# Performance work log

Measured on AMD Instinct MI355X. Metric: run time of the kernel, lower is better.

The kernel has to match this reference:

```python
import jax, jax.numpy as jnp
import numpy as np

N_NODES = 100000
N_EDGES = 1600000
IN_CH = 128
HEADS = 4
OUT_CH = 32
EPS_BN = 1e-5


def setup_inputs() -> dict:
    key = jax.random.key(0)
    ks = jax.random.split(key, 8)
    s = 1.0 / np.sqrt(IN_CH)
    return {
        "x": jax.random.normal(ks[0], (N_NODES, IN_CH), jnp.float32),
        "edge_index": jax.random.randint(ks[1], (2, N_EDGES), 0, N_NODES, jnp.int32),
        "W_src": jax.random.normal(ks[2], (IN_CH, HEADS * OUT_CH), jnp.float32) * s,
        "W_dst": jax.random.normal(ks[3], (IN_CH, HEADS * OUT_CH), jnp.float32) * s,
        "att": jax.random.normal(ks[4], (HEADS, OUT_CH), jnp.float32) * s,
        "bias": jnp.zeros((HEADS * OUT_CH,), jnp.float32),
        "bn_gamma": jnp.ones((HEADS * OUT_CH,), jnp.float32),
        "bn_beta": jnp.zeros((HEADS * OUT_CH,), jnp.float32),
    }


def reference(x, edge_index, W_src, W_dst, att, bias, bn_gamma, bn_beta):
    N = x.shape[0]
    H, C = att.shape
    # add self-loops (PyG default add_self_loops=True)
    loop = jnp.arange(N, dtype=edge_index.dtype)
    src = jnp.concatenate([edge_index[0], loop])  # source j
    dst = jnp.concatenate([edge_index[1], loop])  # destination i

    h_src = (x @ W_src).reshape(N, H, C)
    h_dst = (x @ W_dst).reshape(N, H, C)

    # GATv2 edge scores: a^T LeakyReLU(h_src[j] + h_dst[i]), slope 0.2
    e = jax.nn.leaky_relu(h_src[src] + h_dst[dst], 0.2)  # [E+N, H, C]
    logits = jnp.einsum('ehc,hc->eh', e, att)            # [E+N, H]

    # segment softmax over incoming edges of each destination node
    m = jax.ops.segment_max(logits, dst, num_segments=N)  # [N, H]
    ex = jnp.exp(logits - m[dst])
    denom = jax.ops.segment_sum(ex, dst, num_segments=N)  # [N, H] (>0 via self-loops)
    alpha = ex / denom[dst]                                # [E+N, H]

    # weighted scatter-sum aggregation of source features
    out = jax.ops.segment_sum(alpha[:, :, None] * h_src[src], dst, num_segments=N)
    out = out.reshape(N, H * C) + bias

    # BatchNorm1d (training-mode batch statistics) + LeakyReLU(0.02)
    mean = out.mean(axis=0)
    var = out.var(axis=0)
    y = bn_gamma * (out - mean) * jax.lax.rsqrt(var + EPS_BN) + bn_beta
    return jax.nn.leaky_relu(y, 0.02)
```

## Files before the change

### kernel.cpp

```cpp
#include <hip/hip_runtime.h>
#include <math.h>

#define N_IN   128
#define HC     128
#define HEADS  4
#define PB_T   4096
#define PB_THR 512
#define CAP    8192
#define STB    1024

typedef __attribute__((ext_vector_type(2))) __fp16 f16x2;
typedef __attribute__((ext_vector_type(8))) __fp16 f16x8;
typedef __attribute__((ext_vector_type(4))) float f32x4;

__device__ __forceinline__ unsigned f16pk(float a, float b) {
    f16x2 r = __builtin_amdgcn_cvt_pkrtz(a, b);
    return __builtin_bit_cast(unsigned, r);
}

__global__ __launch_bounds__(256) void k_prep(const float* __restrict__ Ws,
        const float* __restrict__ Wd, unsigned short* __restrict__ Wt) {
    int i = blockIdx.x * 256 + threadIdx.x;
    if (i >= 256 * 128) return;
    int n = i >> 7, k = i & 127;
    float v = (n < 128) ? Ws[k * HC + n] : Wd[k * HC + (n - 128)];
    __fp16 h = (__fp16)v;
    Wt[i] = __builtin_bit_cast(unsigned short, h);
}

__global__ __launch_bounds__(256) void k_gemm(const float* __restrict__ x,
        const __fp16* __restrict__ Wt,
        unsigned short* __restrict__ hs, unsigned short* __restrict__ hd, int N) {
    int wave = threadIdx.x >> 6, lane = threadIdx.x & 63;
    int chbase = wave * 64;
    int nbase = blockIdx.x * 32;
    int lr = lane & 15;
    int lg = lane >> 4;

    f16x8 a[4][4];
#pragma unroll
    for (int ct = 0; ct < 4; ct++)
#pragma unroll
        for (int kk = 0; kk < 4; kk++)
            a[ct][kk] = *reinterpret_cast<const f16x8*>(
                &Wt[(size_t)(chbase + ct * 16 + lr) * 128 + kk * 32 + lg * 8]);

    f32x4 acc[2][4];
#pragma unroll
    for (int rt = 0; rt < 2; rt++)
#pragma unroll
        for (int ct = 0; ct < 4; ct++)
            acc[rt][ct] = (f32x4){0.f, 0.f, 0.f, 0.f};

#pragma unroll
    for (int rt = 0; rt < 2; rt++) {
        int node = nbase + rt * 16 + lr;
        const float* xr = x + (size_t)node * N_IN;
        bool ok = (node < N);
        f16x8 bfr[4];
#pragma unroll
        for (int kk = 0; kk < 4; kk++) {
            f32x4 xa = (f32x4){0.f, 0.f, 0.f, 0.f}, xb = xa;
            if (ok) {
                xa = *reinterpret_cast<const f32x4*>(xr + kk * 32 + lg * 8);
                xb = *reinterpret_cast<const f32x4*>(xr + kk * 32 + lg * 8 + 4);
            }
            uint4 u;
            u.x = f16pk(xa[0], xa[1]); u.y = f16pk(xa[2], xa[3]);
            u.z = f16pk(xb[0], xb[1]); u.w = f16pk(xb[2], xb[3]);
            bfr[kk] = __builtin_bit_cast(f16x8, u);
        }
#pragma unroll
        for (int kk = 0; kk < 4; kk++)
#pragma unroll
            for (int ct = 0; ct < 4; ct++)
                acc[rt][ct] = __builtin_amdgcn_mfma_f32_16x16x32_f16(
                    a[ct][kk], bfr[kk], acc[rt][ct], 0, 0, 0);
    }

#pragma unroll
    for (int rt = 0; rt < 2; rt++) {
        int node = nbase + rt * 16 + lr;
        if (node >= N) continue;
#pragma unroll
        for (int ct = 0; ct < 4; ct++) {
            int ch = chbase + ct * 16 + lg * 4;
            unsigned short* outp = (ch < HC) ? hs : hd;
            int cc = ch & (HC - 1);
            uint2 r;
            r.x = f16pk(acc[rt][ct][0], acc[rt][ct][1]);
            r.y = f16pk(acc[rt][ct][2], acc[rt][ct][3]);
            *reinterpret_cast<uint2*>(outp + (size_t)node * HC + cc) = r;
        }
    }
}

__global__ __launch_bounds__(PB_THR) void k_part(const int* __restrict__ ei,
        int* __restrict__ bcur, unsigned* __restrict__ ebuf, int E, int NB) {
    __shared__ int cnt[512], lscan[512], gbase[512], lcnt[512];
    __shared__ unsigned pr[PB_T];
    __shared__ unsigned short pb[PB_T];
    int t = threadIdx.x;
    int tb = blockIdx.x * PB_T;
    int tc = min(PB_T, E - tb);
    cnt[t] = 0; lcnt[t] = 0;
    __syncthreads();
    int dd[8], ss[8];
#pragma unroll
    for (int i = 0; i < 8; i++) {
        int e = tb + t + i * PB_THR;
        if (e < E) {
            ss[i] = ei[e];
            dd[i] = ei[E + e];
            atomicAdd(&cnt[dd[i] >> 8], 1);
        } else dd[i] = -1;
    }
    __syncthreads();
    lscan[t] = cnt[t];
    __syncthreads();
    for (int ofs = 1; ofs < 512; ofs <<= 1) {
        int add = (t >= ofs) ? lscan[t - ofs] : 0;
        __syncthreads();
        lscan[t] += add;
        __syncthreads();
    }
    if (t < NB && cnt[t] > 0) gbase[t] = atomicAdd(&bcur[t], cnt[t]);
    __syncthreads();
#pragma unroll
    for (int i = 0; i < 8; i++) {
        if (dd[i] >= 0) {
            int b = dd[i] >> 8;
            int lpos = atomicAdd(&lcnt[b], 1);
            int j = lscan[b] - cnt[b] + lpos;
            pr[j] = ((unsigned)ss[i] << 8) | (unsigned)(dd[i] & 255);
            pb[j] = (unsigned short)b;
        }
    }
    __syncthreads();
    for (int k = t; k < tc; k += PB_THR) {
        int b = pb[k];
        ebuf[(size_t)b * CAP + gbase[b] + k - (lscan[b] - cnt[b])] = pr[k];
    }
}

__global__ __launch_bounds__(256) void k_place(const unsigned* __restrict__ ebuf,
        const int* __restrict__ bcur, int* __restrict__ deg, int* __restrict__ off,
        int* __restrict__ ssrc, int N) {
    __shared__ int hist[256], loff[256];
    int b = blockIdx.x;
    int t = threadIdx.x;
    int base = b * CAP;
    int cntb = bcur[b];
    hist[t] = 0;
    __syncthreads();
    for (int k = t; k < cntb; k += 256)
        atomicAdd(&hist[ebuf[base + k] & 255u], 1);
    __syncthreads();
    int v = hist[t];
    loff[t] = v;
    __syncthreads();
    for (int ofs = 1; ofs < 256; ofs <<= 1) {
        int add = (t >= ofs) ? loff[t - ofs] : 0;
        __syncthreads();
        loff[t] += add;
        __syncthreads();
    }
    int excl = loff[t] - v;
    int node = (b << 8) + t;
    if (node < N) { deg[node] = v; off[node] = base + excl; }
    hist[t] = base + excl;
    __syncthreads();
    for (int k = t; k < cntb; k += 256) {
        unsigned u = ebuf[base + k];
        int pos = atomicAdd(&hist[u & 255u], 1);
        ssrc[pos] = (int)(u & 0xFFFFFF00u);
    }
}

__device__ __forceinline__ f16x2 ldh2(const unsigned short* p) {
    return __builtin_bit_cast(f16x2, *reinterpret_cast<const unsigned*>(p));
}
__device__ __forceinline__ f16x2 ldh2o(const unsigned char* b, unsigned o) {
    return __builtin_bit_cast(f16x2, *reinterpret_cast<const unsigned*>(b + o));
}
__device__ __forceinline__ float edge_logit(f16x2 v, f16x2 hdv, f16x2 at2) {
    f16x2 s = v + hdv;
    f16x2 g = s * (f16x2){(__fp16)0.2f, (__fp16)0.2f};
    f16x2 tt = __builtin_elementwise_max(s, g);
    float p = __builtin_amdgcn_fdot2(tt, at2, 0.f, false);
    p += __shfl_xor(p, 1); p += __shfl_xor(p, 2);
    p += __shfl_xor(p, 4); p += __shfl_xor(p, 8);
    return p;
}

__global__ __launch_bounds__(256) void k_agg2(const unsigned short* __restrict__ hs,
        const unsigned short* __restrict__ hd, const int* __restrict__ off,
        const int* __restrict__ deg, const int* __restrict__ ssrc,
        const float* __restrict__ att, unsigned* __restrict__ outh, int N) {
    int wid = (blockIdx.x * 256 + threadIdx.x) >> 6;
    int lane = threadIdx.x & 63;
    if (wid >= N) return;
    int c2 = lane * 2;
    unsigned c4 = (unsigned)lane * 4u;
    const unsigned char* hsb = (const unsigned char*)hs;
    float2 atf = *reinterpret_cast<const float2*>(&att[c2]);
    f16x2 at2 = {(__fp16)atf.x, (__fp16)atf.y};
    f16x2 hdv = ldh2(&hd[(size_t)wid * HC + c2]);
    f16x2 v = ldh2o(hsb, (unsigned)wid * 256u + c4);
    float p = edge_logit(v, hdv, at2);
    float e = __expf(p);
    float ssum = e;
    float2 acc = make_float2(e * (float)v[0], e * (float)v[1]);
    int beg = off[wid], end = beg + deg[wid];
    int i = beg;
    for (; i + 3 < end; i += 4) {
        unsigned o0 = (unsigned)ssrc[i]     + c4;
        unsigned o1 = (unsigned)ssrc[i + 1] + c4;
        unsigned o2 = (unsigned)ssrc[i + 2] + c4;
        unsigned o3 = (unsigned)ssrc[i + 3] + c4;
        f16x2 v0 = ldh2o(hsb, o0);
        f16x2 v1 = ldh2o(hsb, o1);
        f16x2 v2 = ldh2o(hsb, o2);
        f16x2 v3 = ldh2o(hsb, o3);
        float p0 = edge_logit(v0, hdv, at2);
        float p1 = edge_logit(v1, hdv, at2);
        float p2 = edge_logit(v2, hdv, at2);
        float p3 = edge_logit(v3, hdv, at2);
        float e0 = __expf(p0), e1 = __expf(p1);
        float e2 = __expf(p2), e3 = __expf(p3);
        ssum += (e0 + e1) + (e2 + e3);
        acc.x += e0 * (float)v0[0] + e1 * (float)v1[0]
               + e2 * (float)v2[0] + e3 * (float)v3[0];
        acc.y += e0 * (float)v0[1] + e1 * (float)v1[1]
               + e2 * (float)v2[1] + e3 * (float)v3[1];
    }
    for (; i < end; i++) {
        f16x2 ve = ldh2o(hsb, (unsigned)ssrc[i] + c4);
        float pe = edge_logit(ve, hdv, at2);
        float ee = __expf(pe);
        ssum += ee;
        acc.x += ee * (float)ve[0];
        acc.y += ee * (float)ve[1];
    }
    float inv = 1.f / ssum;
    outh[(size_t)wid * 64 + lane] = f16pk(acc.x * inv, acc.y * inv);
}

__global__ __launch_bounds__(256) void k_stats(const unsigned short* __restrict__ outh16,
        float* __restrict__ statp, int N) {
    int ch = threadIdx.x & 127;
    int half = threadIdx.x >> 7;
    float s = 0.f, s2 = 0.f;
    for (int n = blockIdx.x * 2 + half; n < N; n += gridDim.x * 2) {
        __fp16 h = __builtin_bit_cast(__fp16, outh16[(size_t)n * HC + ch]);
        float v = (float)h;
        s += v; s2 += v * v;
    }
    __shared__ float sh[2][256];
    sh[0][threadIdx.x] = s; sh[1][threadIdx.x] = s2;
    __syncthreads();
    if (threadIdx.x < 128) {
        size_t base = (size_t)blockIdx.x * 256;
        statp[base + threadIdx.x]       = sh[0][threadIdx.x] + sh[0][threadIdx.x + 128];
        statp[base + 128 + threadIdx.x] = sh[1][threadIdx.x] + sh[1][threadIdx.x + 128];
    }
}

__global__ __launch_bounds__(256) void k_redstats(const float* __restrict__ statp,
        float* __restrict__ stats, int NBLK) {
    int t = threadIdx.x;
    float acc = 0.f;
    for (int r = blockIdx.x; r < NBLK; r += gridDim.x)
        acc += statp[(size_t)r * 256 + t];
    atomicAdd(&stats[t], acc);
}

__global__ void k_bnparams(const float* __restrict__ stats,
        const float* __restrict__ gamma, const float* __restrict__ beta,
        float* __restrict__ ss, int N) {
    int c = threadIdx.x;
    if (c >= HC) return;
    float mean = stats[c] / (float)N;
    float var  = stats[HC + c] / (float)N - mean * mean;
    float sc = gamma[c] * rsqrtf(var + 1e-5f);
    ss[c]      = sc;
    ss[HC + c] = beta[c] - mean * sc;
}

__global__ __launch_bounds__(256) void k_final(const unsigned short* __restrict__ outh16,
        const float* __restrict__ ss, float* __restrict__ out, int total) {
    int i = blockIdx.x * 256 + threadIdx.x;
    if (i >= total) return;
    int c = i & 127;
    __fp16 h = __builtin_bit_cast(__fp16, outh16[i]);
    float y = (float)h * ss[c] + ss[HC + c];
    out[i] = (y > 0.f) ? y : 0.02f * y;
}

extern "C" void kernel_launch(void* const* d_in, const int* in_sizes, int n_in,
                              void* d_out, int out_size, void* d_ws, size_t ws_size,
                              hipStream_t stream) {
    const float* x     = (const float*)d_in[0];
    const int*   ei    = (const int*)d_in[1];
    const float* Ws    = (const float*)d_in[2];
    const float* Wd    = (const float*)d_in[3];
    const float* att   = (const float*)d_in[4];
    const float* gamma = (const float*)d_in[6];
    const float* beta  = (const float*)d_in[7];
    float* out = (float*)d_out;

    int N  = in_sizes[0] / N_IN;
    int E  = in_sizes[1] / 2;
    int NB = (N + 255) >> 8;

    char* ws = (char*)d_ws;
    unsigned short* hs = (unsigned short*)ws; ws += (size_t)N * HC * 2;
    unsigned short* hd = (unsigned short*)ws; ws += (size_t)N * HC * 2;
    unsigned* outh = (unsigned*)ws; ws += (size_t)N * HC * 2;
    int* deg    = (int*)ws;      ws += (size_t)N * 4;
    int* off    = (int*)ws;      ws += (size_t)N * 4;
    unsigned* ebuf = (unsigned*)ws; ws += (size_t)NB * CAP * 4;
    int* ssrc   = (int*)ws;      ws += (size_t)NB * CAP * 4;
    int* bcur   = (int*)ws;      ws += (size_t)NB * 4;
    unsigned short* Wt = (unsigned short*)ws; ws += 256 * 128 * 2;
    float* statp= (float*)ws;    ws += (size_t)STB * 256 * 4;
    float* stats= (float*)ws;    ws += 2 * HC * 4;
    float* ss   = (float*)ws;    ws += 2 * HC * 4;

    hipMemsetAsync(bcur, 0, (size_t)NB * 4, stream);
    hipMemsetAsync(stats, 0, 2 * HC * 4, stream);

    k_prep<<<128, 256, 0, stream>>>(Ws, Wd, Wt);
    k_gemm<<<(N + 31) / 32, 256, 0, stream>>>(x, (const __fp16*)Wt, hs, hd, N);
    k_part<<<(E + PB_T - 1) / PB_T, PB_THR, 0, stream>>>(ei, bcur, ebuf, E, NB);
    k_place<<<NB, 256, 0, stream>>>(ebuf, bcur, deg, off, ssrc, N);
    k_agg2<<<(N * 64 + 255) / 256, 256, 0, stream>>>(hs, hd, off, deg, ssrc, att, outh, N);
    k_stats<<<STB, 256, 0, stream>>>((const unsigned short*)outh, statp, N);
    k_redstats<<<64, 256, 0, stream>>>(statp, stats, STB);
    k_bnparams<<<1, 128, 0, stream>>>(stats, gamma, beta, ss, N);
    k_final<<<(N * HC + 255) / 256, 256, 0, stream>>>((const unsigned short*)outh, ss, out, N * HC);
}
```

Baseline: 240.2 us.

## Restructure GAT aggregation to split heads across blocks and parallelize edges within wave

```diff
diff --git a/kernel.cpp b/kernel.cpp
--- a/kernel.cpp
+++ b/kernel.cpp
@@ -177,73 +177,95 @@
     }
 }
 
-__device__ __forceinline__ f16x2 ldh2(const unsigned short* p) {
-    return __builtin_bit_cast(f16x2, *reinterpret_cast<const unsigned*>(p));
-}
-__device__ __forceinline__ f16x2 ldh2o(const unsigned char* b, unsigned o) {
-    return __builtin_bit_cast(f16x2, *reinterpret_cast<const unsigned*>(b + o));
-}
-__device__ __forceinline__ float edge_logit(f16x2 v, f16x2 hdv, f16x2 at2) {
-    f16x2 s = v + hdv;
-    f16x2 g = s * (f16x2){(__fp16)0.2f, (__fp16)0.2f};
-    f16x2 tt = __builtin_elementwise_max(s, g);
-    float p = __builtin_amdgcn_fdot2(tt, at2, 0.f, false);
-    p += __shfl_xor(p, 1); p += __shfl_xor(p, 2);
-    p += __shfl_xor(p, 4); p += __shfl_xor(p, 8);
-    return p;
-}
-
 __global__ __launch_bounds__(256) void k_agg2(const unsigned short* __restrict__ hs,
         const unsigned short* __restrict__ hd, const int* __restrict__ off,
         const int* __restrict__ deg, const int* __restrict__ ssrc,
-        const float* __restrict__ att, unsigned* __restrict__ outh, int N) {
-    int wid = (blockIdx.x * 256 + threadIdx.x) >> 6;
+        const float* __restrict__ att, unsigned* __restrict__ outh,
+        int N, int NP) {
+    int b = blockIdx.x;
+    int H = (b >> 2) & 1;
+    int j = (b >> 3) * 4 + (b & 3);
+    int pair = j * 4 + (threadIdx.x >> 6);
+    if (pair >= NP) return;
     int lane = threadIdx.x & 63;
-    if (wid >= N) return;
-    int c2 = lane * 2;
-    unsigned c4 = (unsigned)lane * 4u;
+    int g  = lane >> 5;
+    int e  = (lane >> 3) & 3;
+    int cb = lane & 7;
+    int node = pair * 2 + g;
+    if (node >= N) return;
+
+    unsigned rowoff = (unsigned)(H * 128 + cb * 16);
     const unsigned char* hsb = (const unsigned char*)hs;
-    float2 atf = *reinterpret_cast<const float2*>(&att[c2]);
-    f16x2 at2 = {(__fp16)atf.x, (__fp16)atf.y};
-    f16x2 hdv = ldh2(&hd[(size_t)wid * HC + c2]);
-    f16x2 v = ldh2o(hsb, (unsigned)wid * 256u + c4);
-    float p = edge_logit(v, hdv, at2);
-    float e = __expf(p);
-    float ssum = e;
-    float2 acc = make_float2(e * (float)v[0], e * (float)v[1]);
-    int beg = off[wid], end = beg + deg[wid];
-    int i = beg;
-    for (; i + 3 < end; i += 4) {
-        unsigned o0 = (unsigned)ssrc[i]     + c4;
-        unsigned o1 = (unsigned)ssrc[i + 1] + c4;
-        unsigned o2 = (unsigned)ssrc[i + 2] + c4;
-        unsigned o3 = (unsigned)ssrc[i + 3] + c4;
-        f16x2 v0 = ldh2o(hsb, o0);
-        f16x2 v1 = ldh2o(hsb, o1);
-        f16x2 v2 = ldh2o(hsb, o2);
-        f16x2 v3 = ldh2o(hsb, o3);
-        float p0 = edge_logit(v0, hdv, at2);
-        float p1 = edge_logit(v1, hdv, at2);
-        float p2 = edge_logit(v2, hdv, at2);
-        float p3 = edge_logit(v3, hdv, at2);
-        float e0 = __expf(p0), e1 = __expf(p1);
-        float e2 = __expf(p2), e3 = __expf(p3);
-        ssum += (e0 + e1) + (e2 + e3);
-        acc.x += e0 * (float)v0[0] + e1 * (float)v1[0]
-               + e2 * (float)v2[0] + e3 * (float)v3[0];
-        acc.y += e0 * (float)v0[1] + e1 * (float)v1[1]
-               + e2 * (float)v2[1] + e3 * (float)v3[1];
-    }
-    for (; i < end; i++) {
-        f16x2 ve = ldh2o(hsb, (unsigned)ssrc[i] + c4);
-        float pe = edge_logit(ve, hdv, at2);
-        float ee = __expf(pe);
+    const unsigned char* hdb = (const unsigned char*)hd;
+
+    int chbase = H * 64 + cb * 8;
+    f32x4 a0 = *reinterpret_cast<const f32x4*>(att + chbase);
+    f32x4 a1 = *reinterpret_cast<const f32x4*>(att + chbase + 4);
+    f16x2 at2[4];
+    at2[0] = __builtin_bit_cast(f16x2, f16pk(a0[0], a0[1]));
+    at2[1] = __builtin_bit_cast(f16x2, f16pk(a0[2], a0[3]));
+    at2[2] = __builtin_bit_cast(f16x2, f16pk(a1[0], a1[1]));
+    at2[3] = __builtin_bit_cast(f16x2, f16pk(a1[2], a1[3]));
+
+    uint4 hu = *reinterpret_cast<const uint4*>(hdb + (size_t)node * 256u + rowoff);
+    f16x2 hdv[4];
+    hdv[0] = __builtin_bit_cast(f16x2, hu.x);
+    hdv[1] = __builtin_bit_cast(f16x2, hu.y);
+    hdv[2] = __builtin_bit_cast(f16x2, hu.z);
+    hdv[3] = __builtin_bit_cast(f16x2, hu.w);
+
+    float acc[8];
+#pragma unroll
+    for (int k = 0; k < 8; k++) acc[k] = 0.f;
+    float ssum = 0.f;
+    const f16x2 c02 = {(__fp16)0.2f, (__fp16)0.2f};
+
+    auto process = [&](unsigned byteoff) {
+        uint4 u = *reinterpret_cast<const uint4*>(hsb + byteoff);
+        f16x2 v[4];
+        v[0] = __builtin_bit_cast(f16x2, u.x);
+        v[1] = __builtin_bit_cast(f16x2, u.y);
+        v[2] = __builtin_bit_cast(f16x2, u.z);
+        v[3] = __builtin_bit_cast(f16x2, u.w);
+        float p = 0.f;
+#pragma unroll
+        for (int k = 0; k < 4; k++) {
+            f16x2 s = v[k] + hdv[k];
+            f16x2 t = __builtin_elementwise_max(s, s * c02);
+            p = __builtin_amdgcn_fdot2(t, at2[k], p, false);
+        }
+        p += __shfl_xor(p, 1);
+        p += __shfl_xor(p, 2);
+        float ee = __expf(p);
         ssum += ee;
-        acc.x += ee * (float)ve[0];
-        acc.y += ee * (float)ve[1];
-    }
-    float inv = 1.f / ssum;
-    outh[(size_t)wid * 64 + lane] = f16pk(acc.x * inv, acc.y * inv);
+#pragma unroll
+        for (int k = 0; k < 4; k++) {
+            acc[2 * k]     += ee * (float)v[k][0];
+            acc[2 * k + 1] += ee * (float)v[k][1];
+        }
+    };
+
+    if (e == 0) process((unsigned)node * 256u + rowoff);
+    int beg = off[node], end = beg + deg[node];
+    for (int i = beg + e; i < end; i += 4)
+        process((unsigned)ssrc[i] + rowoff);
+
+    ssum += __shfl_xor(ssum, 8);
+    ssum += __shfl_xor(ssum, 16);
+#pragma unroll
+    for (int k = 0; k < 8; k++) {
+        acc[k] += __shfl_xor(acc[k], 8);
+        acc[k] += __shfl_xor(acc[k], 16);
+    }
+    if (e == 0) {
+        float inv = 1.f / ssum;
+        uint4 r;
+        r.x = f16pk(acc[0] * inv, acc[1] * inv);
+        r.y = f16pk(acc[2] * inv, acc[3] * inv);
+        r.z = f16pk(acc[4] * inv, acc[5] * inv);
+        r.w = f16pk(acc[6] * inv, acc[7] * inv);
+        *reinterpret_cast<uint4*>(outh + (size_t)node * 64 + H * 32 + cb * 4) = r;
+    }
 }
 
 __global__ __launch_bounds__(256) void k_stats(const unsigned short* __restrict__ outh16,
@@ -312,6 +334,9 @@
     int N  = in_sizes[0] / N_IN;
     int E  = in_sizes[1] / 2;
     int NB = (N + 255) >> 8;
+    int NP = (N + 1) / 2;
+    int G4 = (NP + 3) / 4;
+    int AGRID = 8 * ((G4 + 3) / 4);
 
     char* ws = (char*)d_ws;
     unsigned short* hs = (unsigned short*)ws; ws += (size_t)N * HC * 2;
@@ -334,7 +359,7 @@
     k_gemm<<<(N + 31) / 32, 256, 0, stream>>>(x, (const __fp16*)Wt, hs, hd, N);
     k_part<<<(E + PB_T - 1) / PB_T, PB_THR, 0, stream>>>(ei, bcur, ebuf, E, NB);
     k_place<<<NB, 256, 0, stream>>>(ebuf, bcur, deg, off, ssrc, N);
-    k_agg2<<<(N * 64 + 255) / 256, 256, 0, stream>>>(hs, hd, off, deg, ssrc, att, outh, N);
+    k_agg2<<<AGRID, 256, 0, stream>>>(hs, hd, off, deg, ssrc, att, outh, N, NP);
     k_stats<<<STB, 256, 0, stream>>>((const unsigned short*)outh, statp, N);
     k_redstats<<<64, 256, 0, stream>>>(statp, stats, STB);
     k_bnparams<<<1, 128, 0, stream>>>(stats, gamma, beta, ss, N);
```

New measurement: 239.6 us. About the same (-0.2%).
